# Performance work log

Hardware: AMD Instinct MI355X
Metric: run time of the kernel (lower is better)

## Reference

```python
import jax, jax.numpy as jnp
import numpy as np

B, S, K, D = 2, 2048, 8, 1024
P, KP, DFF = 32, 4, 4096


def setup_inputs() -> dict:
    key = jax.random.key(0)
    ks = jax.random.split(key, 17)
    s = 0.02
    return {
        "x": jax.random.normal(ks[0], (B, S, D), jnp.float32),
        "router_out": jax.random.normal(ks[1], (B, S, D), jnp.float32),
        "topk_neuron_idx": jax.random.randint(ks[2], (B, S, K), 0, 512, jnp.int32),
        "topk_neuron_weights": jax.random.uniform(ks[3], (B, S, K), jnp.float32),
        "selected_neurons": jax.random.normal(ks[4], (B, S, K, D), jnp.float32),
        "context": jax.random.normal(ks[5], (B, S, D), jnp.float32),
        "Wq": jax.random.normal(ks[6], (D, D), jnp.float32) * s,
        "bq": jnp.zeros((D,), jnp.float32),
        "Wk": jax.random.normal(ks[7], (D, D), jnp.float32) * s,
        "bk": jnp.zeros((D,), jnp.float32),
        "Wv": jax.random.normal(ks[8], (D, D), jnp.float32) * s,
        "bv": jnp.zeros((D,), jnp.float32),
        "pattern_queries": jax.random.normal(ks[9], (P, D), jnp.float32) * s,
        "Wup": jax.random.normal(ks[10], (DFF, D), jnp.float32) * s,
        "bup": jnp.zeros((DFF,), jnp.float32),
        "Wdown": jax.random.normal(ks[11], (D, DFF), jnp.float32) * s,
        "bdown": jnp.zeros((D,), jnp.float32),
    }


def reference(x, router_out, topk_neuron_idx, topk_neuron_weights,
              selected_neurons, context, Wq, bq, Wk, bk, Wv, bv,
              pattern_queries, Wup, bup, Wdown, bdown):
    scale = 1.0 / jnp.sqrt(jnp.float32(D))
    # K-wide neuron self-attention (per token), torch Linear: y = x @ W.T + b
    q = jnp.einsum('bskd,ed->bske', selected_neurons, Wq) + bq
    kk = jnp.einsum('bskd,ed->bske', selected_neurons, Wk) + bk
    v = jnp.einsum('bskd,ed->bske', selected_neurons, Wv) + bv
    attn = jax.nn.softmax(jnp.einsum('bsqd,bskd->bsqk', q, kk) * scale, axis=-1)
    interacted = jnp.einsum('bsqk,bskd->bsqd', attn, v)  # [B,S,K,D]
    # pattern similarity: [B,S,P,K]
    nps = jnp.einsum('pd,bskd->bspk', pattern_queries, interacted) * scale
    neuron_based = (nps * topk_neuron_weights[:, :, None, :]).sum(-1)  # [B,S,P]
    context_based = jnp.einsum('bsd,pd->bsp', context, pattern_queries)
    pattern_scores = 0.5 * neuron_based + 0.5 * context_based
    topk_scores, topk_idx = jax.lax.top_k(pattern_scores, KP)  # [B,S,KP]
    topk_w = jax.nn.softmax(topk_scores, axis=-1)
    sel_attn = jnp.take_along_axis(nps, topk_idx[..., None], axis=2)  # [B,S,KP,K]
    final_attn = (topk_w[..., None] * jax.nn.softmax(sel_attn, axis=-1)).sum(2)  # [B,S,K]
    aggregated = jnp.einsum('bsk,bskd->bsd', final_attn, interacted)
    combined = x + aggregated
    h = jax.nn.gelu(combined @ Wup.T + bup, approximate=False)
    return h @ Wdown.T + bdown
```

## Files before the change

kernel.cpp:

```cpp
#include <hip/hip_runtime.h>
#include <math.h>

typedef unsigned short ushort_t;
typedef __attribute__((ext_vector_type(8))) short short8;
typedef __attribute__((ext_vector_type(4))) float floatx4;

static __device__ __forceinline__ ushort_t f2bf(float f){
  unsigned int u = __float_as_uint(f);
  unsigned int r = u + 0x7FFFu + ((u >> 16) & 1u);
  return (ushort_t)(r >> 16);
}
static __device__ __forceinline__ void unpack8(uint4 u, float* f){
  f[0] = __uint_as_float(u.x << 16); f[1] = __uint_as_float(u.x & 0xffff0000u);
  f[2] = __uint_as_float(u.y << 16); f[3] = __uint_as_float(u.y & 0xffff0000u);
  f[4] = __uint_as_float(u.z << 16); f[5] = __uint_as_float(u.z & 0xffff0000u);
  f[6] = __uint_as_float(u.w << 16); f[7] = __uint_as_float(u.w & 0xffff0000u);
}
static __device__ __forceinline__ uint4 pack8(const float* f){
  uint4 u;
  u.x = (unsigned)f2bf(f[0]) | ((unsigned)f2bf(f[1]) << 16);
  u.y = (unsigned)f2bf(f[2]) | ((unsigned)f2bf(f[3]) << 16);
  u.z = (unsigned)f2bf(f[4]) | ((unsigned)f2bf(f[5]) << 16);
  u.w = (unsigned)f2bf(f[6]) | ((unsigned)f2bf(f[7]) << 16);
  return u;
}

static __device__ __forceinline__ void gload16(const void* g, void* l){
  __builtin_amdgcn_global_load_lds((const __attribute__((address_space(1))) void*)g,
                                   (__attribute__((address_space(3))) void*)l, 16, 0, 0);
}

static __device__ __forceinline__ float gelu_f(float v){
  float w = v * (-1.5957691216f - 0.0713548162f * v * v);
  return v / (1.0f + __expf(w));
}

__global__ __launch_bounds__(256) void k_cvt_multi(
    const float* __restrict__ s0, ushort_t* __restrict__ d0, int e0,
    const float* __restrict__ s1, ushort_t* __restrict__ d1, int e1,
    const float* __restrict__ s2, ushort_t* __restrict__ d2, int e2,
    const float* __restrict__ s3, ushort_t* __restrict__ d3, int e3,
    const float* __restrict__ s4, ushort_t* __restrict__ d4, int e4,
    const float* __restrict__ s5, ushort_t* __restrict__ d5, int e5){
  int i = blockIdx.x * 256 + threadIdx.x;
  const float* s; ushort_t* d; int b;
  if      (i < e0){ s = s0; d = d0; b = 0;  }
  else if (i < e1){ s = s1; d = d1; b = e0; }
  else if (i < e2){ s = s2; d = d2; b = e1; }
  else if (i < e3){ s = s3; d = d3; b = e2; }
  else if (i < e4){ s = s4; d = d4; b = e3; }
  else if (i < e5){ s = s5; d = d5; b = e4; }
  else return;
  int j = i - b;
  float4 v = ((const float4*)s)[j];
  unsigned long long p = (unsigned long long)f2bf(v.x)
                       | ((unsigned long long)f2bf(v.y) << 16)
                       | ((unsigned long long)f2bf(v.z) << 32)
                       | ((unsigned long long)f2bf(v.w) << 48);
  ((unsigned long long*)d)[j] = p;
}

__global__ __launch_bounds__(256) void k_transpose3(const float* __restrict__ s0, ushort_t* __restrict__ d0,
                                                    const float* __restrict__ s1, ushort_t* __restrict__ d1,
                                                    const float* __restrict__ s2, ushort_t* __restrict__ d2){
  __shared__ float tile[32][33];
  const float* in; ushort_t* out;
  if      (blockIdx.z == 0){ in = s0; out = d0; }
  else if (blockIdx.z == 1){ in = s1; out = d1; }
  else                     { in = s2; out = d2; }
  int bx = blockIdx.x * 32, by = blockIdx.y * 32;
  int tx = threadIdx.x & 31, ty = threadIdx.x >> 5;
  for (int i = 0; i < 32; i += 8)
    tile[ty + i][tx] = in[(size_t)(by + ty + i) * 1024 + bx + tx];
  __syncthreads();
  for (int i = 0; i < 32; i += 8)
    out[(size_t)(bx + ty + i) * 1024 + by + tx] = f2bf(tile[tx][ty + i]);
}

__global__ __launch_bounds__(256) void k_prep(const float* __restrict__ bq,
                                              const ushort_t* __restrict__ WKT,
                                              float* __restrict__ wv,
                                              const float* __restrict__ pat,
                                              const float* __restrict__ bv,
                                              float* __restrict__ pb,
                                              const ushort_t* __restrict__ WVT,
                                              const ushort_t* __restrict__ PATB,
                                              ushort_t* __restrict__ PVB,
                                              const ushort_t* __restrict__ CTXB,
                                              float* __restrict__ CBb){
  __shared__ ushort_t As[128 * 32];
  __shared__ ushort_t Bs[32 * 32];
  const int bid = blockIdx.x;
  const int l = threadIdx.x & 63;
  if (bid < 256){
    int d = (bid << 2) + (threadIdx.x >> 6);
    const uint4* row = (const uint4*)(WKT + (size_t)d * 1024 + (l << 4));
    const float4* b4 = (const float4*)(bq + (l << 4));
    float w[16], bb[16];
    unpack8(row[0], w); unpack8(row[1], w + 8);
#pragma unroll
    for (int i = 0; i < 4; i++){
      float4 v = b4[i];
      bb[i*4] = v.x; bb[i*4+1] = v.y; bb[i*4+2] = v.z; bb[i*4+3] = v.w;
    }
    float a = 0.f;
#pragma unroll
    for (int i = 0; i < 16; i++) a += w[i] * bb[i];
#pragma unroll
    for (int s = 1; s < 64; s <<= 1) a += __shfl_xor(a, s);
    if (l == 0) wv[d] = a;
  } else if (bid < 264){
    int p = ((bid - 256) << 2) + (threadIdx.x >> 6);
    const float4* pr = (const float4*)(pat + p * 1024) + l;
    const float4* b4 = (const float4*)bv + l;
    float a = 0.f;
#pragma unroll
    for (int i = 0; i < 4; i++){
      float4 x = pr[i * 64], y = b4[i * 64];
      a += x.x * y.x + x.y * y.y + x.z * y.z + x.w * y.w;
    }
#pragma unroll
    for (int s = 1; s < 64; s <<= 1) a += __shfl_xor(a, s);
    if (l == 0) pb[p] = a;
  } else if (bid < 520){
    int d = ((bid - 264) << 2) + (threadIdx.x >> 6);
    const uint4* wr = (const uint4*)(WVT + (size_t)d * 1024 + (l << 4));
    float w[16];
    unpack8(wr[0], w); unpack8(wr[1], w + 8);
    for (int p = 0; p < 32; p++){
      const uint4* pr = (const uint4*)(PATB + p * 1024 + (l << 4));
      float pw[16];
      unpack8(pr[0], pw); unpack8(pr[1], pw + 8);
      float a = 0.f;
#pragma unroll
      for (int i = 0; i < 16; i++) a += w[i] * pw[i];
#pragma unroll
      for (int s = 1; s < 64; s <<= 1) a += __shfl_xor(a, s);
      if (l == 0) PVB[p * 1024 + d] = f2bf(a);
    }
  } else {
    const int tid = threadIdx.x;
    const int w = tid >> 6;
    const int m0 = (bid - 520) << 7;
    const int rA = (w << 4) + (l >> 2);
    const int cA = (l & 3) << 3;
    const int fr = l & 15, fq = l >> 4;
    const int K = 1024;
    floatx4 acc[2][2];
#pragma unroll
    for (int i = 0; i < 2; i++)
#pragma unroll
      for (int j = 0; j < 2; j++) acc[i][j] = (floatx4)0.0f;
    const ushort_t* Ab = CTXB + (size_t)(m0 + rA) * K + cA;
    const ushort_t* Bb = PATB + (size_t)rA * K + cA;
    const size_t row64 = (size_t)64 * K;
    for (int k0 = 0; k0 < K; k0 += 32){
      __syncthreads();
      gload16(Ab + k0, As + (w << 9));
      gload16(Ab + row64 + k0, As + 2048 + (w << 9));
      if (w < 2) gload16(Bb + k0, Bs + (w << 9));
      __syncthreads();
      short8 af[2], bg[2];
#pragma unroll
      for (int i = 0; i < 2; i++)
        af[i] = *(const short8*)(As + (((w << 5) + (i << 4) + fr) << 5) + (fq << 3));
#pragma unroll
      for (int j = 0; j < 2; j++)
        bg[j] = *(const short8*)(Bs + (((j << 4) + fr) << 5) + (fq << 3));
#pragma unroll
      for (int i = 0; i < 2; i++)
#pragma unroll
        for (int j = 0; j < 2; j++)
          acc[i][j] = __builtin_amdgcn_mfma_f32_16x16x32_bf16(af[i], bg[j], acc[i][j], 0, 0, 0);
    }
#pragma unroll
    for (int i = 0; i < 2; i++){
      int row = m0 + (w << 5) + (i << 4) + (fq << 2);
#pragma unroll
      for (int j = 0; j < 2; j++){
        int col = (j << 4) + fr;
#pragma unroll
        for (int r = 0; r < 4; r++)
          CBb[(size_t)(row + r) * 32 + col] = acc[i][j][r];
      }
    }
  }
}

#define SBAR_  __builtin_amdgcn_s_barrier()
#define SCHED_ __builtin_amdgcn_sched_barrier(0)
#define LGKM0_ asm volatile("s_waitcnt lgkmcnt(0)" ::: "memory")
#define VM4_   asm volatile("s_waitcnt vmcnt(4)" ::: "memory")
#define VM2_   asm volatile("s_waitcnt vmcnt(2)" ::: "memory")
#define VM0_   asm volatile("s_waitcnt vmcnt(0)" ::: "memory")

#define STG_(Gp, Lp, qh, tt) do{ \
    const ushort_t* _g = (Gp) + (size_t)(((qh) << 7) + (wid << 3)) * K + ((tt) << 6); \
    char* _l = (Lp) + ((((tt) & 1) << 15) | ((qh) << 14) | (wid << 10)); \
    gload16(_g, _l); \
    gload16(_g + ((size_t)K << 6), _l + 8192); \
  }while(0)

#define RDA_(qm, cb) do{ \
    _Pragma("unroll") \
    for (int _i = 0; _i < 4; _i++){ \
      af[_i][0] = *(const short8*)(AsB + (cb) + ((qm) << 14) + arow + (_i << 11) + c0); \
      af[_i][1] = *(const short8*)(AsB + (cb) + ((qm) << 14) + arow + (_i << 11) + c1); \
    } }while(0)

#define RDB_(qn, cb) do{ \
    _Pragma("unroll") \
    for (int _j = 0; _j < 2; _j++){ \
      bg[qn][_j][0] = *(const short8*)(BsB + (cb) + ((qn) << 14) + brow + (_j << 11) + c0); \
      bg[qn][_j][1] = *(const short8*)(BsB + (cb) + ((qn) << 14) + brow + (_j << 11) + c1); \
    } }while(0)

#define MFMA_(qm, qn) do{ \
    _Pragma("unroll") \
    for (int _i = 0; _i < 4; _i++) \
    _Pragma("unroll") \
      for (int _j = 0; _j < 2; _j++){ \
        acc[qm][_i][qn][_j] = __builtin_amdgcn_mfma_f32_16x16x32_bf16(af[_i][0], bg[qn][_j][0], acc[qm][_i][qn][_j], 0, 0, 0); \
        acc[qm][_i][qn][_j] = __builtin_amdgcn_mfma_f32_16x16x32_bf16(af[_i][1], bg[qn][_j][1], acc[qm][_i][qn][_j], 0, 0, 0); \
      } }while(0)

template<int MODE>
__global__ __launch_bounds__(512, 2) void k_gemm8(const ushort_t* __restrict__ A,
                                                  const ushort_t* __restrict__ B,
                                                  void* __restrict__ C,
                                                  const float* __restrict__ bias,
                                                  int N, int K, int ntn){
  __shared__ __align__(16) ushort_t As[2 * 256 * 64];
  __shared__ __align__(16) ushort_t Bs[2 * 256 * 64];
  const int tid = threadIdx.x;
  const int wid = tid >> 6, l = tid & 63;
  const int wr = wid >> 2, wc = wid & 3;
  const int fr = l & 15, fq = l >> 4;
  const int id = blockIdx.x;
  const int xcd = id & 7, t2 = id >> 3;
  const int nt = t2 % ntn, mq = t2 / ntn;
  const int mt = (mq << 3) + xcd;
  const int m0 = mt << 8, n0 = nt << 8;
  const int NT = K >> 6;

  const int sgr = l >> 3;
  const int sgc = ((l & 7) ^ (l >> 3)) << 3;
  const ushort_t* Ag = A + (size_t)(m0 + sgr) * K + sgc;
  const ushort_t* Bg = B + (size_t)(n0 + sgr) * K + sgc;
  char* AsB = (char*)As;
  char* BsB = (char*)Bs;
  const int c0 = ((fq ^ (fr & 7)) << 4);
  const int c1 = (((4 | fq) ^ (fr & 7)) << 4);
  const int arow = (wr << 13) + fr * 128;
  const int brow = (wc << 12) + fr * 128;

  floatx4 acc[2][4][2][2];
#pragma unroll
  for (int a = 0; a < 2; a++)
#pragma unroll
    for (int b = 0; b < 4; b++)
#pragma unroll
      for (int c = 0; c < 2; c++)
#pragma unroll
        for (int d = 0; d < 2; d++) acc[a][b][c][d] = (floatx4)0.0f;
  short8 af[4][2], bg[2][2][2];

  STG_(Ag, AsB, 0, 0);
  STG_(Bg, BsB, 0, 0);
  STG_(Bg, BsB, 1, 0);
  STG_(Ag, AsB, 1, 0);
  VM4_; SBAR_;

  for (int t = 0; t < NT - 1; t++){
    const int cur = (t & 1) << 15;
    const int tn = t + 1;
    RDA_(0, cur); RDB_(0, cur);
    STG_(Ag, AsB, 0, tn);
    SCHED_; SBAR_; LGKM0_; SCHED_;
    __builtin_amdgcn_s_setprio(1); MFMA_(0, 0); __builtin_amdgcn_s_setprio(0);
    SCHED_; VM4_; SBAR_;
    RDB_(1, cur);
    STG_(Bg, BsB, 0, tn);
    SCHED_; SBAR_; LGKM0_; SCHED_;
    __builtin_amdgcn_s_setprio(1); MFMA_(0, 1); __builtin_amdgcn_s_setprio(0);
    SCHED_; VM4_; SBAR_;
    RDA_(1, cur);
    STG_(Bg, BsB, 1, tn);
    SCHED_; SBAR_; LGKM0_; SCHED_;
    __builtin_amdgcn_s_setprio(1); MFMA_(1, 1); __builtin_amdgcn_s_setprio(0);
    SCHED_; SBAR_;
    STG_(Ag, AsB, 1, tn);
    SCHED_; SBAR_; SCHED_;
    __builtin_amdgcn_s_setprio(1); MFMA_(1, 0); __builtin_amdgcn_s_setprio(0);
    SCHED_; VM4_; SBAR_;
  }
  {
    const int cur = ((NT - 1) & 1) << 15;
    RDA_(0, cur); RDB_(0, cur);
    SCHED_; SBAR_; LGKM0_; SCHED_;
    __builtin_amdgcn_s_setprio(1); MFMA_(0, 0); __builtin_amdgcn_s_setprio(0);
    SCHED_; VM2_; SBAR_;
    RDB_(1, cur);
    SCHED_; SBAR_; LGKM0_; SCHED_;
    __builtin_amdgcn_s_setprio(1); MFMA_(0, 1); __builtin_amdgcn_s_setprio(0);
    SCHED_; VM0_; SBAR_;
    RDA_(1, cur);
    SCHED_; SBAR_; LGKM0_; SCHED_;
    __builtin_amdgcn_s_setprio(1); MFMA_(1, 1); MFMA_(1, 0); __builtin_amdgcn_s_setprio(0);
  }

#pragma unroll
  for (int qm = 0; qm < 2; qm++)
#pragma unroll
    for (int i = 0; i < 4; i++){
      const int row = m0 + (qm << 7) + (wr << 6) + (i << 4) + (fq << 2);
#pragma unroll
      for (int qn = 0; qn < 2; qn++)
#pragma unroll
        for (int j = 0; j < 2; j++){
          const int col = n0 + (qn << 7) + (wc << 5) + (j << 4) + fr;
          const float bsv = bias[col];
#pragma unroll
          for (int r = 0; r < 4; r++){
            float v = acc[qm][i][qn][j][r] + bsv;
            if (MODE == 3) v = gelu_f(v);
            ((ushort_t*)C)[(size_t)(row + r) * N + col] = f2bf(v);
          }
        }
    }
}

template<int MODE, int GN>
__global__ __launch_bounds__(256) void k_gemm_bt64(const ushort_t* __restrict__ A,
                                                   const ushort_t* __restrict__ B,
                                                   void* __restrict__ C,
                                                   const float* __restrict__ bias,
                                                   const float* __restrict__ Xadd,
                                                   int N, int K){
  __shared__ ushort_t As[2 * 64 * 32];
  __shared__ ushort_t Bs[2 * 128 * 32];
  const int tid = threadIdx.x;
  const int w = tid >> 6, l = tid & 63;
  const int id = blockIdx.x;
  const int xcd = id & 7;
  const int t2 = id >> 3;
  const int nmq = (int)(gridDim.x >> 3) / GN;
  const int nt = t2 / nmq;
  const int mq = t2 - nt * nmq;
  const int mt = (mq << 3) + xcd;
  const int m0 = mt << 6, n0 = nt << 7;
  const int wm = (w >> 1) << 5, wn = (w & 1) << 6;
  const int rA = (w << 4) + (l >> 2);
  const int cA = (l & 3) << 3;
  const int fr = l & 15, fq = l >> 4;

  floatx4 acc[2][4];
#pragma unroll
  for (int i = 0; i < 2; i++)
#pragma unroll
    for (int j = 0; j < 4; j++) acc[i][j] = (floatx4)0.0f;

  const ushort_t* Ab = A + (size_t)(m0 + rA) * K + cA;
  const ushort_t* Bb = B + (size_t)(n0 + rA) * K + cA;
  const size_t row64 = (size_t)64 * K;

  for (int k0 = 0; k0 < K; k0 += 64){
    __syncthreads();
    gload16(Ab + k0, As + (w << 9));
    gload16(Ab + k0 + 32, As + 2048 + (w << 9));
    gload16(Bb + k0, Bs + (w << 9));
    gload16(Bb + row64 + k0, Bs + 2048 + (w << 9));
    gload16(Bb + k0 + 32, Bs + 4096 + (w << 9));
    gload16(Bb + row64 + k0 + 32, Bs + 6144 + (w << 9));
    __syncthreads();
#pragma unroll
    for (int h = 0; h < 2; h++){
      const ushort_t* Ah = As + (h << 11);
      const ushort_t* Bh = Bs + (h << 12);
      short8 af[2], bg[4];
#pragma unroll
      for (int i = 0; i < 2; i++)
        af[i] = *(const short8*)(Ah + ((wm + (i << 4) + fr) << 5) + (fq << 3));
#pragma unroll
      for (int j = 0; j < 4; j++)
        bg[j] = *(const short8*)(Bh + ((wn + (j << 4) + fr) << 5) + (fq << 3));
#pragma unroll
      for (int i = 0; i < 2; i++)
#pragma unroll
        for (int j = 0; j < 4; j++)
          acc[i][j] = __builtin_amdgcn_mfma_f32_16x16x32_bf16(af[i], bg[j], acc[i][j], 0, 0, 0);
    }
  }

#pragma unroll
  for (int i = 0; i < 2; i++){
    int row = m0 + wm + (i << 4) + (fq << 2);
#pragma unroll
    for (int j = 0; j < 4; j++){
      int col = n0 + wn + (j << 4) + fr;
      float b = (MODE >= 2) ? bias[col] : 0.0f;
#pragma unroll
      for (int r = 0; r < 4; r++){
        float v = acc[i][j][r] + b;
        size_t idx = (size_t)(row + r) * N + col;
        if (MODE == 2) v += Xadd[idx];
        if (MODE == 4) ((float*)C)[idx] = v;
        else           ((ushort_t*)C)[idx] = f2bf(v);
      }
    }
  }
}

__global__ __launch_bounds__(256) void k_attn(const ushort_t* __restrict__ T,
                                              const ushort_t* __restrict__ SNB,
                                              const ushort_t* __restrict__ PVB,
                                              const float* __restrict__ PBv,
                                              const float* __restrict__ CB,
                                              const float* __restrict__ TW,
                                              ushort_t* __restrict__ GSN){
  __shared__ float logit_s[4 * 256];
  __shared__ float attn_s[8 * 64];
  __shared__ float npr_s[8 * 256];
  __shared__ float nps_s[8 * 256];
  __shared__ float sc_s[8 * 32];
  __shared__ float tw_s[8 * 8];
  __shared__ float pb_s[32];
  __shared__ int   sel_s[8 * 4];
  __shared__ float tkw_s[8 * 4], rmax_s[8 * 4], rsum_s[8 * 4], fa_s[8 * 8], g_s[8 * 8];

  const int t = threadIdx.x;
  const int w = t >> 6, l = t & 63;
  const int tok0 = blockIdx.x << 3;
  const int pair = (blockIdx.x << 2) + w;

  {
    const size_t rbase = (size_t)pair * 16 + (l & 15);
    const int ko = (l >> 4) << 3;
    const ushort_t* Ap = T   + rbase * 1024 + ko;
    const ushort_t* Bp = SNB + rbase * 1024 + ko;
    const ushort_t* P0 = PVB + (size_t)(l & 15) * 1024 + ko;
    const ushort_t* P1 = P0 + 16 * 1024;
    floatx4 aL = (floatx4)0.0f, aP0 = (floatx4)0.0f, aP1 = (floatx4)0.0f;
#pragma unroll 4
    for (int k0 = 0; k0 < 1024; k0 += 32){
      short8 b = *(const short8*)(Bp + k0);
      aL  = __builtin_amdgcn_mfma_f32_16x16x32_bf16(*(const short8*)(Ap + k0), b, aL, 0, 0, 0);
      aP0 = __builtin_amdgcn_mfma_f32_16x16x32_bf16(*(const short8*)(P0 + k0), b, aP0, 0, 0, 0);
      aP1 = __builtin_amdgcn_mfma_f32_16x16x32_bf16(*(const short8*)(P1 + k0), b, aP1, 0, 0, 0);
    }
    const int col = l & 15, r0 = (l >> 4) << 2;
#pragma unroll
    for (int r = 0; r < 4; r++)
      logit_s[(w << 8) + (r0 + r) * 16 + col] = aL[r] * 0.03125f;
    const int tokloc = (w << 1) + (col >> 3), kk = col & 7;
#pragma unroll
    for (int r = 0; r < 4; r++){
      npr_s[(tokloc << 8) + kk * 32 + (r0 + r)]      = aP0[r];
      npr_s[(tokloc << 8) + kk * 32 + (r0 + r) + 16] = aP1[r];
    }
  }
  if (t < 64) tw_s[t] = TW[(tok0 << 3) + t];
  if (t < 32) pb_s[t] = PBv[t];
  __syncthreads();

  const int loc = t >> 5, q = t & 31;
  if (q < 8){
    const float* lrow = logit_s + ((loc >> 1) << 8) + (loc & 1) * 136 + q * 16;
    float a[8]; float m = -1e30f;
#pragma unroll
    for (int j = 0; j < 8; j++){ a[j] = lrow[j]; m = fmaxf(m, a[j]); }
    float s = 0.f;
#pragma unroll
    for (int j = 0; j < 8; j++){ a[j] = expf(a[j] - m); s += a[j]; }
    float inv = 1.f / s;
#pragma unroll
    for (int j = 0; j < 8; j++) attn_s[(loc << 6) + q * 8 + j] = a[j] * inv;
  }
  __syncthreads();

  {
    const int qq = q & 7, p0 = (q >> 3) << 3;
    float a[8];
#pragma unroll
    for (int k = 0; k < 8; k++) a[k] = attn_s[(loc << 6) + qq * 8 + k];
    const float* np = npr_s + (loc << 8);
    float* npsr = nps_s + (loc << 8);
    for (int p = p0; p < p0 + 8; p++){
      float acc = pb_s[p];
#pragma unroll
      for (int k = 0; k < 8; k++) acc += a[k] * np[k * 32 + p];
      npsr[p * 8 + qq] = acc * 0.03125f;
    }
  }
  __syncthreads();

  {
    const float* npsr = nps_s + (loc << 8);
    float nb = 0.f;
#pragma unroll
    for (int qq = 0; qq < 8; qq++) nb += npsr[q * 8 + qq] * tw_s[(loc << 3) + qq];
    sc_s[(loc << 5) + q] = 0.5f * nb + 0.5f * CB[((size_t)(tok0 + loc) << 5) + q];
  }
  __syncthreads();

  if (q == 0){
    const float* sc = sc_s + (loc << 5);
    unsigned used = 0; float vals[4]; int idx[4];
    for (int kp = 0; kp < 4; kp++){
      float best = -1e30f; int bi = 0;
      for (int p = 0; p < 32; p++)
        if (!((used >> p) & 1u) && sc[p] > best){ best = sc[p]; bi = p; }
      used |= 1u << bi; vals[kp] = best; idx[kp] = bi;
    }
    float mm = vals[0], ss = 0.f, e[4];
    for (int kp = 0; kp < 4; kp++){ e[kp] = expf(vals[kp] - mm); ss += e[kp]; }
    for (int kp = 0; kp < 4; kp++){ tkw_s[(loc << 2) + kp] = e[kp] / ss; sel_s[(loc << 2) + kp] = idx[kp]; }
  }
  __syncthreads();

  if (q < 4){
    const float* npsr = nps_s + (loc << 8);
    int p = sel_s[(loc << 2) + q];
    float mm = -1e30f;
    for (int j = 0; j < 8; j++) mm = fmaxf(mm, npsr[p * 8 + j]);
    float ss = 0.f;
    for (int j = 0; j < 8; j++) ss += expf(npsr[p * 8 + j] - mm);
    rmax_s[(loc << 2) + q] = mm; rsum_s[(loc << 2) + q] = ss;
  }
  __syncthreads();

  if (q < 8){
    const float* npsr = nps_s + (loc << 8);
    float f = 0.f;
    for (int kp = 0; kp < 4; kp++){
      int p = sel_s[(loc << 2) + kp];
      f += tkw_s[(loc << 2) + kp] * expf(npsr[p * 8 + q] - rmax_s[(loc << 2) + kp]) / rsum_s[(loc << 2) + kp];
    }
    fa_s[(loc << 3) + q] = f;
  }
  __syncthreads();

  if (q < 8){
    float g = 0.f;
    for (int qq = 0; qq < 8; qq++) g += fa_s[(loc << 3) + qq] * attn_s[(loc << 6) + qq * 8 + q];
    g_s[(loc << 3) + q] = g;
  }
  __syncthreads();

  for (int tl = 0; tl < 2; tl++){
    const int tkl = (w << 1) + tl;
    const size_t tok = (size_t)tok0 + tkl;
    float o[16];
#pragma unroll
    for (int i = 0; i < 16; i++) o[i] = 0.f;
#pragma unroll
    for (int k = 0; k < 8; k++){
      float gk = g_s[(tkl << 3) + k];
      const uint4* src = (const uint4*)(SNB + ((tok << 3) + k) * 1024 + (l << 4));
      float f0[8], f1[8];
      unpack8(src[0], f0);
      unpack8(src[1], f1);
#pragma unroll
      for (int i = 0; i < 8; i++){ o[i] += gk * f0[i]; o[8 + i] += gk * f1[i]; }
    }
    uint4* dst = (uint4*)(GSN + tok * 1024 + (l << 4));
    dst[0] = pack8(o);
    dst[1] = pack8(o + 8);
  }
}

extern "C" void kernel_launch(void* const* d_in, const int* in_sizes, int n_in,
                              void* d_out, int out_size, void* d_ws, size_t ws_size,
                              hipStream_t stream){
  (void)in_sizes; (void)n_in; (void)out_size; (void)ws_size;
  const float* x   = (const float*)d_in[0];
  const float* tw  = (const float*)d_in[3];
  const float* SN  = (const float*)d_in[4];
  const float* ctx = (const float*)d_in[5];
  const float* Wq  = (const float*)d_in[6];
  const float* bq  = (const float*)d_in[7];
  const float* Wk  = (const float*)d_in[8];
  const float* Wv  = (const float*)d_in[10];
  const float* bv  = (const float*)d_in[11];
  const float* pat = (const float*)d_in[12];
  const float* Wup = (const float*)d_in[13];
  const float* bup = (const float*)d_in[14];
  const float* Wdn = (const float*)d_in[15];
  const float* bdn = (const float*)d_in[16];
  float* out = (float*)d_out;

  char* ws = (char*)d_ws;
  size_t off = 0;
  auto alloc = [&](size_t bytes) -> char* {
    char* p = ws + off;
    off = (off + bytes + 255) & ~(size_t)255;
    return p;
  };
  ushort_t* SNB  = (ushort_t*)alloc(67108864);
  ushort_t* TB   = (ushort_t*)alloc(67108864);
  float*    CBb  = (float*)alloc(524288);
  ushort_t* GSN  = (ushort_t*)alloc(8388608);
  ushort_t* CTXB = (ushort_t*)alloc(8388608);
  ushort_t* PATB = (ushort_t*)alloc(65536);
  ushort_t* WVB  = (ushort_t*)alloc(2097152);
  ushort_t* WUPB = (ushort_t*)alloc(8388608);
  ushort_t* WDNB = (ushort_t*)alloc(8388608);
  ushort_t* ATB  = (ushort_t*)alloc(2097152);
  ushort_t* WKTB = (ushort_t*)alloc(2097152);
  ushort_t* WQTB = (ushort_t*)alloc(2097152);
  ushort_t* WVTB = (ushort_t*)alloc(2097152);
  ushort_t* PVB  = (ushort_t*)alloc(65536);
  float*    WVEC = (float*)alloc(4096);
  float*    PBv  = (float*)alloc(128);
  ushort_t* H    = SNB;
  ushort_t* CMB  = TB;

  const int e0 = 8388608, e1 = e0 + 1048576, e2 = e1 + 8192,
            e3 = e2 + 262144, e4 = e3 + 1048576, e5 = e4 + 1048576;
  k_cvt_multi<<<(e5 + 255) / 256, 256, 0, stream>>>(
      SN, SNB, e0, ctx, CTXB, e1, pat, PATB, e2,
      Wv, WVB, e3, Wup, WUPB, e4, Wdn, WDNB, e5);
  k_transpose3<<<dim3(32, 32, 3), 256, 0, stream>>>(Wq, WQTB, Wk, WKTB, Wv, WVTB);
  k_prep<<<552, 256, 0, stream>>>(bq, WKTB, WVEC, pat, bv, PBv, WVTB, PATB, PVB, CTXB, CBb);

  k_gemm_bt64<0, 8><<<128, 256, 0, stream>>>(WKTB, WQTB, ATB, nullptr, nullptr, 1024, 1024);
  k_gemm8<1><<<512, 512, 0, stream>>>(SNB, ATB, TB, WVEC, 1024, 1024, 4);
  k_attn<<<512, 256, 0, stream>>>(TB, SNB, PVB, PBv, CBb, tw, GSN);
  k_gemm_bt64<2, 8><<<512, 256, 0, stream>>>(GSN, WVB, CMB, bv, x, 1024, 1024);
  k_gemm8<3><<<256, 512, 0, stream>>>(CMB, WUPB, H, bup, 4096, 1024, 16);
  k_gemm_bt64<4, 8><<<512, 256, 0, stream>>>(H, WDNB, out, bdn, nullptr, 1024, 4096);
}
```

Measured before the change: 557.9 us.

## Simplify GEMM main loop to issue all next-tile loads up front

Replaces the finely interleaved four-phase ping-pong schedule (staggered global-to-LDS loads, barriers, lgkmcnt waits and setprio around each MFMA quadrant) with a simpler loop. Each iteration issues all four next-tile loads at once, waits for the current tile, takes a single barrier, then runs all four MFMA quadrants back to back. This cuts the number of barriers and explicit waits per iteration and lets the compiler schedule LDS reads against MFMAs. The cost is losing the hand-tuned overlap and wave priority control, and the vmcnt(8) count must match the number of loads STG_ actually issues.

```diff
diff --git a/kernel.cpp b/kernel.cpp
--- a/kernel.cpp
+++ b/kernel.cpp
@@ -189,9 +189,7 @@
 
 #define SBAR_  __builtin_amdgcn_s_barrier()
 #define SCHED_ __builtin_amdgcn_sched_barrier(0)
-#define LGKM0_ asm volatile("s_waitcnt lgkmcnt(0)" ::: "memory")
-#define VM4_   asm volatile("s_waitcnt vmcnt(4)" ::: "memory")
-#define VM2_   asm volatile("s_waitcnt vmcnt(2)" ::: "memory")
+#define VM8_   asm volatile("s_waitcnt vmcnt(8)" ::: "memory")
 #define VM0_   asm volatile("s_waitcnt vmcnt(0)" ::: "memory")
 
 #define STG_(Gp, Lp, qh, tt) do{ \
@@ -269,44 +267,28 @@
   STG_(Bg, BsB, 0, 0);
   STG_(Bg, BsB, 1, 0);
   STG_(Ag, AsB, 1, 0);
-  VM4_; SBAR_;
-
-  for (int t = 0; t < NT - 1; t++){
+
+  for (int t = 0; t < NT; t++){
     const int cur = (t & 1) << 15;
     const int tn = t + 1;
+    if (tn < NT){
+      STG_(Ag, AsB, 0, tn);
+      STG_(Bg, BsB, 0, tn);
+      STG_(Bg, BsB, 1, tn);
+      STG_(Ag, AsB, 1, tn);
+      VM8_;
+    } else {
+      VM0_;
+    }
+    SBAR_; SCHED_;
     RDA_(0, cur); RDB_(0, cur);
-    STG_(Ag, AsB, 0, tn);
-    SCHED_; SBAR_; LGKM0_; SCHED_;
-    __builtin_amdgcn_s_setprio(1); MFMA_(0, 0); __builtin_amdgcn_s_setprio(0);
-    SCHED_; VM4_; SBAR_;
+    MFMA_(0, 0);
     RDB_(1, cur);
-    STG_(Bg, BsB, 0, tn);
-    SCHED_; SBAR_; LGKM0_; SCHED_;
-    __builtin_amdgcn_s_setprio(1); MFMA_(0, 1); __builtin_amdgcn_s_setprio(0);
-    SCHED_; VM4_; SBAR_;
+    MFMA_(0, 1);
     RDA_(1, cur);
-    STG_(Bg, BsB, 1, tn);
-    SCHED_; SBAR_; LGKM0_; SCHED_;
-    __builtin_amdgcn_s_setprio(1); MFMA_(1, 1); __builtin_amdgcn_s_setprio(0);
+    MFMA_(1, 1);
+    MFMA_(1, 0);
     SCHED_; SBAR_;
-    STG_(Ag, AsB, 1, tn);
-    SCHED_; SBAR_; SCHED_;
-    __builtin_amdgcn_s_setprio(1); MFMA_(1, 0); __builtin_amdgcn_s_setprio(0);
-    SCHED_; VM4_; SBAR_;
-  }
-  {
-    const int cur = ((NT - 1) & 1) << 15;
-    RDA_(0, cur); RDB_(0, cur);
-    SCHED_; SBAR_; LGKM0_; SCHED_;
-    __builtin_amdgcn_s_setprio(1); MFMA_(0, 0); __builtin_amdgcn_s_setprio(0);
-    SCHED_; VM2_; SBAR_;
-    RDB_(1, cur);
-    SCHED_; SBAR_; LGKM0_; SCHED_;
-    __builtin_amdgcn_s_setprio(1); MFMA_(0, 1); __builtin_amdgcn_s_setprio(0);
-    SCHED_; VM0_; SBAR_;
-    RDA_(1, cur);
-    SCHED_; SBAR_; LGKM0_; SCHED_;
-    __builtin_amdgcn_s_setprio(1); MFMA_(1, 1); MFMA_(1, 0); __builtin_amdgcn_s_setprio(0);
   }
 
 #pragma unroll
```

Measured after the change: 566.2 us. About the same (+1.5%).

## Merge convert/transpose launches and fold WK^T·WQ GEMM into prep kernel

Applied to the files above, without the earlier changes.

The bf16 conversion and the three weight transposes now run in a single launch, with a block-index split deciding which job each block does. The small 1024x1024 WK^T·WQ product moves out of its own GEMM launch and into k_prep as 128 extra blocks with a simple 64x128 MFMA tile. The aim is to cut launch and tail overhead on the preprocessing path. The main GEMM loop also drops several sched_barriers and adds unroll 2, which hands the compiler more freedom to interleave instructions but could upset the hand-tuned schedule.

```diff
diff --git a/kernel.cpp b/kernel.cpp
--- a/kernel.cpp
+++ b/kernel.cpp
@@ -35,40 +35,45 @@
   return v / (1.0f + __expf(w));
 }
 
-__global__ __launch_bounds__(256) void k_cvt_multi(
+__global__ __launch_bounds__(256) void k_cvt_tr(
     const float* __restrict__ s0, ushort_t* __restrict__ d0, int e0,
     const float* __restrict__ s1, ushort_t* __restrict__ d1, int e1,
     const float* __restrict__ s2, ushort_t* __restrict__ d2, int e2,
     const float* __restrict__ s3, ushort_t* __restrict__ d3, int e3,
     const float* __restrict__ s4, ushort_t* __restrict__ d4, int e4,
-    const float* __restrict__ s5, ushort_t* __restrict__ d5, int e5){
-  int i = blockIdx.x * 256 + threadIdx.x;
-  const float* s; ushort_t* d; int b;
-  if      (i < e0){ s = s0; d = d0; b = 0;  }
-  else if (i < e1){ s = s1; d = d1; b = e0; }
-  else if (i < e2){ s = s2; d = d2; b = e1; }
-  else if (i < e3){ s = s3; d = d3; b = e2; }
-  else if (i < e4){ s = s4; d = d4; b = e3; }
-  else if (i < e5){ s = s5; d = d5; b = e4; }
-  else return;
-  int j = i - b;
-  float4 v = ((const float4*)s)[j];
-  unsigned long long p = (unsigned long long)f2bf(v.x)
-                       | ((unsigned long long)f2bf(v.y) << 16)
-                       | ((unsigned long long)f2bf(v.z) << 32)
-                       | ((unsigned long long)f2bf(v.w) << 48);
-  ((unsigned long long*)d)[j] = p;
-}
-
-__global__ __launch_bounds__(256) void k_transpose3(const float* __restrict__ s0, ushort_t* __restrict__ d0,
-                                                    const float* __restrict__ s1, ushort_t* __restrict__ d1,
-                                                    const float* __restrict__ s2, ushort_t* __restrict__ d2){
+    const float* __restrict__ s5, ushort_t* __restrict__ d5, int e5,
+    const float* __restrict__ t0, ushort_t* __restrict__ u0,
+    const float* __restrict__ t1, ushort_t* __restrict__ u1,
+    const float* __restrict__ t2, ushort_t* __restrict__ u2,
+    int cvt_blocks){
   __shared__ float tile[32][33];
+  const int bid = blockIdx.x;
+  if (bid < cvt_blocks){
+    int i = bid * 256 + threadIdx.x;
+    const float* s; ushort_t* d; int b;
+    if      (i < e0){ s = s0; d = d0; b = 0;  }
+    else if (i < e1){ s = s1; d = d1; b = e0; }
+    else if (i < e2){ s = s2; d = d2; b = e1; }
+    else if (i < e3){ s = s3; d = d3; b = e2; }
+    else if (i < e4){ s = s4; d = d4; b = e3; }
+    else if (i < e5){ s = s5; d = d5; b = e4; }
+    else return;
+    int j = i - b;
+    float4 v = ((const float4*)s)[j];
+    unsigned long long p = (unsigned long long)f2bf(v.x)
+                         | ((unsigned long long)f2bf(v.y) << 16)
+                         | ((unsigned long long)f2bf(v.z) << 32)
+                         | ((unsigned long long)f2bf(v.w) << 48);
+    ((unsigned long long*)d)[j] = p;
+    return;
+  }
+  const int tb = bid - cvt_blocks;
+  const int z = tb >> 10, rem = tb & 1023;
+  const int by = (rem >> 5) << 5, bx = (rem & 31) << 5;
   const float* in; ushort_t* out;
-  if      (blockIdx.z == 0){ in = s0; out = d0; }
-  else if (blockIdx.z == 1){ in = s1; out = d1; }
-  else                     { in = s2; out = d2; }
-  int bx = blockIdx.x * 32, by = blockIdx.y * 32;
+  if      (z == 0){ in = t0; out = u0; }
+  else if (z == 1){ in = t1; out = u1; }
+  else            { in = t2; out = u2; }
   int tx = threadIdx.x & 31, ty = threadIdx.x >> 5;
   for (int i = 0; i < 32; i += 8)
     tile[ty + i][tx] = in[(size_t)(by + ty + i) * 1024 + bx + tx];
@@ -87,9 +92,11 @@
                                               const ushort_t* __restrict__ PATB,
                                               ushort_t* __restrict__ PVB,
                                               const ushort_t* __restrict__ CTXB,
-                                              float* __restrict__ CBb){
+                                              float* __restrict__ CBb,
+                                              const ushort_t* __restrict__ WQT,
+                                              ushort_t* __restrict__ ATBo){
   __shared__ ushort_t As[128 * 32];
-  __shared__ ushort_t Bs[32 * 32];
+  __shared__ ushort_t Bs[2 * 128 * 32];
   const int bid = blockIdx.x;
   const int l = threadIdx.x & 63;
   if (bid < 256){
@@ -138,7 +145,7 @@
       for (int s = 1; s < 64; s <<= 1) a += __shfl_xor(a, s);
       if (l == 0) PVB[p * 1024 + d] = f2bf(a);
     }
-  } else {
+  } else if (bid < 552){
     const int tid = threadIdx.x;
     const int w = tid >> 6;
     const int m0 = (bid - 520) << 7;
@@ -182,6 +189,65 @@
 #pragma unroll
         for (int r = 0; r < 4; r++)
           CBb[(size_t)(row + r) * 32 + col] = acc[i][j][r];
+      }
+    }
+  } else {
+    const int tid = threadIdx.x;
+    const int w = tid >> 6;
+    const int id = bid - 552;
+    const int xcd = id & 7, t2 = id >> 3;
+    const int nt = t2 >> 1, mq = t2 & 1;
+    const int mt = (mq << 3) + xcd;
+    const int m0 = mt << 6, n0 = nt << 7;
+    const int wm = (w >> 1) << 5, wn = (w & 1) << 6;
+    const int rA = (w << 4) + (l >> 2);
+    const int cA = (l & 3) << 3;
+    const int fr = l & 15, fq = l >> 4;
+    const int K = 1024, N = 1024;
+    floatx4 acc[2][4];
+#pragma unroll
+    for (int i = 0; i < 2; i++)
+#pragma unroll
+      for (int j = 0; j < 4; j++) acc[i][j] = (floatx4)0.0f;
+    const ushort_t* Ab = WKT + (size_t)(m0 + rA) * K + cA;
+    const ushort_t* Bb = WQT + (size_t)(n0 + rA) * K + cA;
+    const size_t row64 = (size_t)64 * K;
+    for (int k0 = 0; k0 < K; k0 += 64){
+      __syncthreads();
+      gload16(Ab + k0, As + (w << 9));
+      gload16(Ab + k0 + 32, As + 2048 + (w << 9));
+      gload16(Bb + k0, Bs + (w << 9));
+      gload16(Bb + row64 + k0, Bs + 2048 + (w << 9));
+      gload16(Bb + k0 + 32, Bs + 4096 + (w << 9));
+      gload16(Bb + row64 + k0 + 32, Bs + 6144 + (w << 9));
+      __syncthreads();
+#pragma unroll
+      for (int h = 0; h < 2; h++){
+        const ushort_t* Ah = As + (h << 11);
+        const ushort_t* Bh = Bs + (h << 12);
+        short8 af[2], bg[4];
+#pragma unroll
+        for (int i = 0; i < 2; i++)
+          af[i] = *(const short8*)(Ah + ((wm + (i << 4) + fr) << 5) + (fq << 3));
+#pragma unroll
+        for (int j = 0; j < 4; j++)
+          bg[j] = *(const short8*)(Bh + ((wn + (j << 4) + fr) << 5) + (fq << 3));
+#pragma unroll
+        for (int i = 0; i < 2; i++)
+#pragma unroll
+          for (int j = 0; j < 4; j++)
+            acc[i][j] = __builtin_amdgcn_mfma_f32_16x16x32_bf16(af[i], bg[j], acc[i][j], 0, 0, 0);
+      }
+    }
+#pragma unroll
+    for (int i = 0; i < 2; i++){
+      int row = m0 + wm + (i << 4) + (fq << 2);
+#pragma unroll
+      for (int j = 0; j < 4; j++){
+        int col = n0 + wn + (j << 4) + fr;
+#pragma unroll
+        for (int r = 0; r < 4; r++)
+          ATBo[(size_t)(row + r) * N + col] = f2bf(acc[i][j][r]);
       }
     }
   }
@@ -271,41 +337,42 @@
   STG_(Ag, AsB, 1, 0);
   VM4_; SBAR_;
 
+#pragma unroll 2
   for (int t = 0; t < NT - 1; t++){
     const int cur = (t & 1) << 15;
     const int tn = t + 1;
     RDA_(0, cur); RDB_(0, cur);
     STG_(Ag, AsB, 0, tn);
-    SCHED_; SBAR_; LGKM0_; SCHED_;
+    SBAR_; LGKM0_; SCHED_;
     __builtin_amdgcn_s_setprio(1); MFMA_(0, 0); __builtin_amdgcn_s_setprio(0);
-    SCHED_; VM4_; SBAR_;
+    VM4_; SBAR_;
     RDB_(1, cur);
     STG_(Bg, BsB, 0, tn);
-    SCHED_; SBAR_; LGKM0_; SCHED_;
+    SBAR_; LGKM0_; SCHED_;
     __builtin_amdgcn_s_setprio(1); MFMA_(0, 1); __builtin_amdgcn_s_setprio(0);
-    SCHED_; VM4_; SBAR_;
+    VM4_; SBAR_;
     RDA_(1, cur);
     STG_(Bg, BsB, 1, tn);
-    SCHED_; SBAR_; LGKM0_; SCHED_;
+    SBAR_; LGKM0_; SCHED_;
     __builtin_amdgcn_s_setprio(1); MFMA_(1, 1); __builtin_amdgcn_s_setprio(0);
-    SCHED_; SBAR_;
+    SBAR_;
     STG_(Ag, AsB, 1, tn);
-    SCHED_; SBAR_; SCHED_;
+    SBAR_;
     __builtin_amdgcn_s_setprio(1); MFMA_(1, 0); __builtin_amdgcn_s_setprio(0);
-    SCHED_; VM4_; SBAR_;
+    VM4_; SBAR_;
   }
   {
     const int cur = ((NT - 1) & 1) << 15;
     RDA_(0, cur); RDB_(0, cur);
-    SCHED_; SBAR_; LGKM0_; SCHED_;
+    SBAR_; LGKM0_; SCHED_;
     __builtin_amdgcn_s_setprio(1); MFMA_(0, 0); __builtin_amdgcn_s_setprio(0);
-    SCHED_; VM2_; SBAR_;
+    VM2_; SBAR_;
     RDB_(1, cur);
-    SCHED_; SBAR_; LGKM0_; SCHED_;
+    SBAR_; LGKM0_; SCHED_;
     __builtin_amdgcn_s_setprio(1); MFMA_(0, 1); __builtin_amdgcn_s_setprio(0);
-    SCHED_; VM0_; SBAR_;
+    VM0_; SBAR_;
     RDA_(1, cur);
-    SCHED_; SBAR_; LGKM0_; SCHED_;
+    SBAR_; LGKM0_; SCHED_;
     __builtin_amdgcn_s_setprio(1); MFMA_(1, 1); MFMA_(1, 0); __builtin_amdgcn_s_setprio(0);
   }
 
@@ -617,13 +684,14 @@
 
   const int e0 = 8388608, e1 = e0 + 1048576, e2 = e1 + 8192,
             e3 = e2 + 262144, e4 = e3 + 1048576, e5 = e4 + 1048576;
-  k_cvt_multi<<<(e5 + 255) / 256, 256, 0, stream>>>(
+  const int cvtb = (e5 + 255) / 256;
+  k_cvt_tr<<<cvtb + 3072, 256, 0, stream>>>(
       SN, SNB, e0, ctx, CTXB, e1, pat, PATB, e2,
-      Wv, WVB, e3, Wup, WUPB, e4, Wdn, WDNB, e5);
-  k_transpose3<<<dim3(32, 32, 3), 256, 0, stream>>>(Wq, WQTB, Wk, WKTB, Wv, WVTB);
-  k_prep<<<552, 256, 0, stream>>>(bq, WKTB, WVEC, pat, bv, PBv, WVTB, PATB, PVB, CTXB, CBb);
-
-  k_gemm_bt64<0, 8><<<128, 256, 0, stream>>>(WKTB, WQTB, ATB, nullptr, nullptr, 1024, 1024);
+      Wv, WVB, e3, Wup, WUPB, e4, Wdn, WDNB, e5,
+      Wq, WQTB, Wk, WKTB, Wv, WVTB, cvtb);
+  k_prep<<<680, 256, 0, stream>>>(bq, WKTB, WVEC, pat, bv, PBv, WVTB, PATB, PVB,
+                                  CTXB, CBb, WQTB, ATB);
+
   k_gemm8<1><<<512, 512, 0, stream>>>(SNB, ATB, TB, WVEC, 1024, 1024, 4);
   k_attn<<<512, 256, 0, stream>>>(TB, SNB, PVB, PBv, CBb, tw, GSN);
   k_gemm_bt64<2, 8><<<512, 256, 0, stream>>>(GSN, WVB, CMB, bv, x, 1024, 1024);
```

Result: faster. 541.5 us (-2.9%).
